# Performance work log

Measured on AMD Instinct MI355X. Metric: run time of the kernel, lower is better.

Reference implementation:

```python
import jax, jax.numpy as jnp
import numpy as np

N = 60000          # users
M = 40000          # items
NODES = N + M
D = 64             # embedding_dim
NLAYERS = 3        # layers = [64, 64, 64]
NNZ = 3_200_000    # nnz of L_I (avg degree 32)
B = 1024           # batch_size
NEG_SLOPE = 0.2


def setup_inputs() -> dict:
    key = jax.random.key(0)
    ks = jax.random.split(key, 12)
    edge_row = jax.random.randint(ks[0], (NNZ,), 0, NODES, dtype=jnp.int32)
    edge_col = jax.random.randint(ks[1], (NNZ,), 0, NODES, dtype=jnp.int32)
    # Laplacian values are small positive normalized weights
    edge_val = jax.random.uniform(ks[2], (NNZ,), dtype=jnp.float32) * (1.0 / 32.0)
    embed_user = jax.random.normal(ks[3], (N, D), dtype=jnp.float32) * 0.1
    embed_item = jax.random.normal(ks[4], (M, D), dtype=jnp.float32) * 0.1
    W1 = jax.random.normal(ks[5], (NLAYERS, D, D), dtype=jnp.float32) * 0.1
    W2 = jax.random.normal(ks[6], (NLAYERS, D, D), dtype=jnp.float32) * 0.1
    b1 = jax.random.normal(ks[7], (NLAYERS, 1, D), dtype=jnp.float32) * 0.1
    b2 = jax.random.normal(ks[8], (NLAYERS, 1, D), dtype=jnp.float32) * 0.1
    sampled_users = jax.random.randint(ks[9], (B,), 0, N, dtype=jnp.int32)
    observed_items_idx = jax.random.randint(ks[10], (B,), 0, M, dtype=jnp.int32)
    unobserved_items_idx = jax.random.randint(ks[11], (B,), 0, M, dtype=jnp.int32)
    return {
        "edge_row": edge_row, "edge_col": edge_col, "edge_val": edge_val,
        "embed_user": embed_user, "embed_item": embed_item,
        "W1": W1, "W2": W2, "b1": b1, "b2": b2,
        "sampled_users": sampled_users,
        "observed_items_idx": observed_items_idx,
        "unobserved_items_idx": unobserved_items_idx,
    }


def _spmm(row, col, val, x):
    # sparse (NODES x NODES) @ dense (NODES x D) via gather + segment-sum
    return jax.ops.segment_sum(val[:, None] * x[col], row, num_segments=NODES)


def reference(edge_row, edge_col, edge_val, embed_user, embed_item,
              W1, W2, b1, b2,
              sampled_users, observed_items_idx, unobserved_items_idx):
    x = jnp.concatenate([embed_user, embed_item], axis=0)  # (NODES, D)
    reprs = [x]
    for i in range(NLAYERS):
        lie = _spmm(edge_row, edge_col, edge_val, x)        # L_I @ E
        left = lie @ W1[i] + b1[i]
        right = (x * lie) @ W2[i] + b2[i]
        x = jax.nn.leaky_relu(left + right, negative_slope=NEG_SLOPE)
        reprs.append(x)
    final_reprs = jnp.concatenate(reprs, axis=1)            # (NODES, D*(NLAYERS+1))
    users_, items_ = final_reprs[:N], final_reprs[N:]
    return (users_[sampled_users],
            items_[observed_items_idx],
            items_[unobserved_items_idx])
```

## Files before the change

kernel.cpp:

```cpp
#include <hip/hip_runtime.h>

#define NN    60000
#define NODES 100000
#define DD    64
#define NNZ   3200000
#define BB    1024
#define NEG   0.2f
#define RPB   256
#define NBUCK 391
#define EPB   8192
#define NPB   ((NNZ + EPB - 1) / EPB)
#define CAP   8960
#define BCAP  9216

__global__ __launch_bounds__(256) void k_init_x(const float* __restrict__ eu,
                                                const float* __restrict__ ei,
                                                float* __restrict__ x,
                                                int* __restrict__ gcur) {
    int i = blockIdx.x * 256 + threadIdx.x;
    if (i < NBUCK) gcur[i] = i * CAP;
    const int TOT = NODES * DD / 4;
    if (i >= TOT) return;
    const int UE = NN * DD / 4;
    float4 v = (i < UE) ? ((const float4*)eu)[i] : ((const float4*)ei)[i - UE];
    ((float4*)x)[i] = v;
}

__global__ __launch_bounds__(512) void k_place(const int* __restrict__ row,
                                               const int* __restrict__ col,
                                               const float* __restrict__ val,
                                               int* __restrict__ gcur,
                                               int2* __restrict__ bulk) {
    __shared__ int rows_l[EPB];
    __shared__ unsigned short perm[EPB];
    __shared__ int h[NBUCK], bloc[NBUCK], bcur[NBUCK], gseg[NBUCK];
    __shared__ int sc[512];
    int t = threadIdx.x;
    if (t < NBUCK) h[t] = 0;
    __syncthreads();
    int base = blockIdx.x * EPB;
    int n = min(EPB, NNZ - base);
    for (int k = t; k < n; k += 512) {
        int r = row[base + k];
        rows_l[k] = r;
        atomicAdd(&h[r >> 8], 1);
    }
    __syncthreads();
    {
        int v = (t < NBUCK) ? h[t] : 0;
        sc[t] = v;
        __syncthreads();
        for (int off = 1; off < 512; off <<= 1) {
            int u = (t >= off) ? sc[t - off] : 0;
            __syncthreads();
            sc[t] += u;
            __syncthreads();
        }
        if (t < NBUCK) {
            int ex = sc[t] - v;
            bloc[t] = ex;
            bcur[t] = ex;
            gseg[t] = v ? atomicAdd(&gcur[t], v) : 0;
        }
    }
    __syncthreads();
    for (int k = t; k < n; k += 512) {
        int p = atomicAdd(&bcur[rows_l[k] >> 8], 1);
        perm[p] = (unsigned short)k;
    }
    __syncthreads();
    for (int j = t; j < n; j += 512) {
        int k = perm[j];
        int r = rows_l[k];
        int b8 = r >> 8;
        int addr = gseg[b8] + (j - bloc[b8]);
        bulk[addr] = make_int2(((r & 255) << 17) | col[base + k],
                               __float_as_int(val[base + k]));
    }
}

__global__ __launch_bounds__(512) void k_csr(const int* __restrict__ gcur,
                                             int2* __restrict__ bulk,
                                             int2* __restrict__ rsd) {
    __shared__ int2 eds[BCAP];
    __shared__ int h[RPB], sc[RPB], bcur[RPB];
    int b = blockIdx.x, t = threadIdx.x;
    int lo = b * CAP;
    int n = gcur[b] - lo;
    if (t < RPB) h[t] = 0;
    __syncthreads();
    for (int i = t; i < n; i += 512) {
        int2 ed = bulk[lo + i];
        eds[i] = ed;
        atomicAdd(&h[ed.x >> 17], 1);
    }
    __syncthreads();
    int v = 0;
    if (t < RPB) { v = h[t]; sc[t] = v; }
    __syncthreads();
    for (int off = 1; off < RPB; off <<= 1) {
        int u = 0;
        if (t < RPB && t >= off) u = sc[t - off];
        __syncthreads();
        if (t < RPB) sc[t] += u;
        __syncthreads();
    }
    if (t < RPB) {
        int ex = sc[t] - v;
        bcur[t] = ex;
        int r = b * RPB + t;
        if (r < NODES) rsd[r] = make_int2(lo + ex, lo + ex + v);
    }
    __syncthreads();
    for (int i = t; i < n; i += 512) {
        int2 ed = eds[i];
        int p = atomicAdd(&bcur[ed.x >> 17], 1);
        bulk[lo + p] = make_int2(ed.x & 0x1FFFF, ed.y);
    }
}

__global__ __launch_bounds__(256) void k_spmm(const int2* __restrict__ rsd,
                                              const int2* __restrict__ cv,
                                              const float* __restrict__ x,
                                              float* __restrict__ lie) {
    int w    = (blockIdx.x * 256 + threadIdx.x) >> 6;
    int lane = threadIdx.x & 63;
    if (w >= NODES) return;
    int2 se = rsd[w];
    int s = se.x, e = se.y;
    float acc = 0.f;
    int g = s;
    for (; g + 16 <= e; g += 16) {
        int2 ee[16];
#pragma unroll
        for (int j = 0; j < 16; ++j) ee[j] = cv[g + j];
        float xv[16];
#pragma unroll
        for (int j = 0; j < 16; ++j) xv[j] = x[ee[j].x * DD + lane];
#pragma unroll
        for (int j = 0; j < 16; ++j) acc = fmaf(__int_as_float(ee[j].y), xv[j], acc);
    }
    for (; g + 8 <= e; g += 8) {
        int2 ee[8];
#pragma unroll
        for (int j = 0; j < 8; ++j) ee[j] = cv[g + j];
        float xv[8];
#pragma unroll
        for (int j = 0; j < 8; ++j) xv[j] = x[ee[j].x * DD + lane];
#pragma unroll
        for (int j = 0; j < 8; ++j) acc = fmaf(__int_as_float(ee[j].y), xv[j], acc);
    }
    for (; g < e; ++g) {
        int2 ed = cv[g];
        acc = fmaf(__int_as_float(ed.y), x[ed.x * DD + lane], acc);
    }
    lie[w * DD + lane] = acc;
}

__global__ __launch_bounds__(256) void k_gemm(float* __restrict__ x,
                                              const float* __restrict__ lie,
                                              const float* __restrict__ W1,
                                              const float* __restrict__ W2,
                                              const float* __restrict__ b1,
                                              const float* __restrict__ b2) {
    __shared__ float A1[64 * 64];
    __shared__ float A2[64 * 64];
    __shared__ float Ws1[64 * 64];
    __shared__ float Ws2[64 * 64];

    const int t = threadIdx.x;
    const int row0 = blockIdx.x * 64;

    {
        const float4* w1v = (const float4*)W1;
        const float4* w2v = (const float4*)W2;
        float4* s1v = (float4*)Ws1;
        float4* s2v = (float4*)Ws2;
#pragma unroll
        for (int q = 0; q < 4; ++q) {
            s1v[q * 256 + t] = w1v[q * 256 + t];
            s2v[q * 256 + t] = w2v[q * 256 + t];
        }
    }
#pragma unroll
    for (int q = 0; q < 4; ++q) {
        int f4 = q * 256 + t;
        int rl = f4 >> 4;
        int c4 = f4 & 15;
        int gr = row0 + rl;
        float4 lv = make_float4(0.f, 0.f, 0.f, 0.f);
        float4 xv = make_float4(0.f, 0.f, 0.f, 0.f);
        if (gr < NODES) {
            lv = *(const float4*)&lie[gr * DD + c4 * 4];
            xv = *(const float4*)&x[gr * DD + c4 * 4];
        }
        int sg = c4 ^ (rl & 15);
        ((float4*)A1)[rl * 16 + sg] = lv;
        ((float4*)A2)[rl * 16 + sg] = make_float4(lv.x * xv.x, lv.y * xv.y,
                                                  lv.z * xv.z, lv.w * xv.w);
    }
    __syncthreads();

    const int tx = t & 15;
    const int ty = t >> 4;
    float bs[4];
    {
        float4 bb1 = *(const float4*)&b1[tx * 4];
        float4 bb2 = *(const float4*)&b2[tx * 4];
        bs[0] = bb1.x + bb2.x; bs[1] = bb1.y + bb2.y;
        bs[2] = bb1.z + bb2.z; bs[3] = bb1.w + bb2.w;
    }
    float acc[4][4];
#pragma unroll
    for (int i = 0; i < 4; ++i)
#pragma unroll
        for (int j = 0; j < 4; ++j) acc[i][j] = bs[j];

    for (int k4 = 0; k4 < 16; ++k4) {
        float4 a1[4], a2[4];
#pragma unroll
        for (int i = 0; i < 4; ++i) {
            int r = ty * 4 + i;
            int sg = k4 ^ (r & 15);
            a1[i] = ((const float4*)A1)[r * 16 + sg];
            a2[i] = ((const float4*)A2)[r * 16 + sg];
        }
#pragma unroll
        for (int kk = 0; kk < 4; ++kk) {
            float4 w1 = ((const float4*)Ws1)[(k4 * 4 + kk) * 16 + tx];
            float4 w2 = ((const float4*)Ws2)[(k4 * 4 + kk) * 16 + tx];
#pragma unroll
            for (int i = 0; i < 4; ++i) {
                float av1 = (&a1[i].x)[kk];
                float av2 = (&a2[i].x)[kk];
                acc[i][0] = fmaf(av1, w1.x, fmaf(av2, w2.x, acc[i][0]));
                acc[i][1] = fmaf(av1, w1.y, fmaf(av2, w2.y, acc[i][1]));
                acc[i][2] = fmaf(av1, w1.z, fmaf(av2, w2.z, acc[i][2]));
                acc[i][3] = fmaf(av1, w1.w, fmaf(av2, w2.w, acc[i][3]));
            }
        }
    }
#pragma unroll
    for (int i = 0; i < 4; ++i) {
        int gr = row0 + ty * 4 + i;
        if (gr < NODES) {
            float4 o;
            o.x = acc[i][0] >= 0.f ? acc[i][0] : NEG * acc[i][0];
            o.y = acc[i][1] >= 0.f ? acc[i][1] : NEG * acc[i][1];
            o.z = acc[i][2] >= 0.f ? acc[i][2] : NEG * acc[i][2];
            o.w = acc[i][3] >= 0.f ? acc[i][3] : NEG * acc[i][3];
            *(float4*)&x[gr * DD + tx * 4] = o;
        }
    }
}

__global__ __launch_bounds__(256) void k_gather(const float* __restrict__ x,
                                                const int* __restrict__ su,
                                                const int* __restrict__ oi,
                                                const int* __restrict__ ui,
                                                float* __restrict__ out, int layer) {
    int w    = (blockIdx.x * 256 + threadIdx.x) >> 6;
    int lane = threadIdx.x & 63;
    if (w >= 3 * BB) return;
    int g = w >> 10, b = w & 1023;
    int node = (g == 0) ? su[b] : (NN + ((g == 1) ? oi[b] : ui[b]));
    out[w * 256 + layer * 64 + lane] = x[node * DD + lane];
}

extern "C" void kernel_launch(void* const* d_in, const int* in_sizes, int n_in,
                              void* d_out, int out_size, void* d_ws, size_t ws_size,
                              hipStream_t stream) {
    const int*   edge_row = (const int*)d_in[0];
    const int*   edge_col = (const int*)d_in[1];
    const float* edge_val = (const float*)d_in[2];
    const float* eu = (const float*)d_in[3];
    const float* ei = (const float*)d_in[4];
    const float* W1 = (const float*)d_in[5];
    const float* W2 = (const float*)d_in[6];
    const float* b1 = (const float*)d_in[7];
    const float* b2 = (const float*)d_in[8];
    const int*   su = (const int*)d_in[9];
    const int*   oi = (const int*)d_in[10];
    const int*   ui = (const int*)d_in[11];
    float* out = (float*)d_out;

    float* x    = (float*)d_ws;
    float* lie  = x + NODES * DD;
    int2*  bulk = (int2*)(lie + NODES * DD);
    int*   gcur = (int*)(bulk + NBUCK * CAP);
    int2*  rsd  = (int2*)(gcur + NBUCK + 1);

    k_init_x<<<(NODES * DD / 4 + 255) / 256, 256, 0, stream>>>(eu, ei, x, gcur);
    k_gather<<<(3 * BB * 64 + 255) / 256, 256, 0, stream>>>(x, su, oi, ui, out, 0);

    k_place<<<NPB, 512, 0, stream>>>(edge_row, edge_col, edge_val, gcur, bulk);
    k_csr<<<NBUCK, 512, 0, stream>>>(gcur, bulk, rsd);

    for (int l = 0; l < 3; ++l) {
        k_spmm<<<(NODES * 64 + 255) / 256, 256, 0, stream>>>(rsd, bulk, x, lie);
        k_gemm<<<(NODES + 63) / 64, 256, 0, stream>>>(x, lie,
                                                      W1 + l * 4096, W2 + l * 4096,
                                                      b1 + l * 64,  b2 + l * 64);
        k_gather<<<(3 * BB * 64 + 255) / 256, 256, 0, stream>>>(x, su, oi, ui, out, l + 1);
    }
}
```

Measured before the change: 610.7 us.

## Sort edges by column segment within row buckets for cache-local SpMM gathers

Rows are bucketed into 196-row groups, and inside each bucket edges are sorted by (column segment of 8192 nodes, local row). A new block-per-bucket SpMM kernel walks the 13 column segments in order and accumulates partial row sums in shared memory. All blocks then gather from the same slice of x at roughly the same time, which should improve L2 hit rates. The cost is more per-key overhead, since each segment holds only short runs of about 2-3 edges, and only 511 large blocks are launched, which may limit occupancy and latency hiding.

```diff
diff --git a/kernel.cpp b/kernel.cpp
--- a/kernel.cpp
+++ b/kernel.cpp
@@ -6,12 +6,15 @@
 #define NNZ   3200000
 #define BB    1024
 #define NEG   0.2f
-#define RPB   256
-#define NBUCK 391
+#define RPB   196
+#define NBUCK 511
 #define EPB   8192
 #define NPB   ((NNZ + EPB - 1) / EPB)
-#define CAP   8960
-#define BCAP  9216
+#define CAP   7000
+#define BCAP  7168
+#define NSEG  13
+#define KEYN  (NSEG * RPB)
+#define SPB   (KEYN + 1)
 
 __global__ __launch_bounds__(256) void k_init_x(const float* __restrict__ eu,
                                                 const float* __restrict__ ei,
@@ -43,7 +46,7 @@
     for (int k = t; k < n; k += 512) {
         int r = row[base + k];
         rows_l[k] = r;
-        atomicAdd(&h[r >> 8], 1);
+        atomicAdd(&h[r / RPB], 1);
     }
     __syncthreads();
     {
@@ -65,96 +68,111 @@
     }
     __syncthreads();
     for (int k = t; k < n; k += 512) {
-        int p = atomicAdd(&bcur[rows_l[k] >> 8], 1);
+        int p = atomicAdd(&bcur[rows_l[k] / RPB], 1);
         perm[p] = (unsigned short)k;
     }
     __syncthreads();
     for (int j = t; j < n; j += 512) {
         int k = perm[j];
         int r = rows_l[k];
-        int b8 = r >> 8;
-        int addr = gseg[b8] + (j - bloc[b8]);
-        bulk[addr] = make_int2(((r & 255) << 17) | col[base + k],
+        int b = r / RPB;
+        int addr = gseg[b] + (j - bloc[b]);
+        bulk[addr] = make_int2(((r - b * RPB) << 17) | col[base + k],
                                __float_as_int(val[base + k]));
     }
 }
 
 __global__ __launch_bounds__(512) void k_csr(const int* __restrict__ gcur,
                                              int2* __restrict__ bulk,
-                                             int2* __restrict__ rsd) {
+                                             int* __restrict__ starts) {
     __shared__ int2 eds[BCAP];
-    __shared__ int h[RPB], sc[RPB], bcur[RPB];
+    __shared__ int cnt[KEYN], pos[KEYN];
+    __shared__ int part[512];
     int b = blockIdx.x, t = threadIdx.x;
     int lo = b * CAP;
     int n = gcur[b] - lo;
-    if (t < RPB) h[t] = 0;
+    for (int k = t; k < KEYN; k += 512) cnt[k] = 0;
     __syncthreads();
     for (int i = t; i < n; i += 512) {
         int2 ed = bulk[lo + i];
         eds[i] = ed;
-        atomicAdd(&h[ed.x >> 17], 1);
-    }
-    __syncthreads();
-    int v = 0;
-    if (t < RPB) { v = h[t]; sc[t] = v; }
-    __syncthreads();
-    for (int off = 1; off < RPB; off <<= 1) {
-        int u = 0;
-        if (t < RPB && t >= off) u = sc[t - off];
+        int lr = ed.x >> 17, c = ed.x & 0x1FFFF;
+        atomicAdd(&cnt[(c >> 13) * RPB + lr], 1);
+    }
+    __syncthreads();
+    int run = 0;
+#pragma unroll
+    for (int j = 0; j < 5; ++j) {
+        int k = t * 5 + j;
+        if (k < KEYN) { pos[k] = run; run += cnt[k]; }
+    }
+    part[t] = run;
+    __syncthreads();
+    for (int off = 1; off < 512; off <<= 1) {
+        int u = (t >= off) ? part[t - off] : 0;
         __syncthreads();
-        if (t < RPB) sc[t] += u;
+        part[t] += u;
         __syncthreads();
     }
-    if (t < RPB) {
-        int ex = sc[t] - v;
-        bcur[t] = ex;
-        int r = b * RPB + t;
-        if (r < NODES) rsd[r] = make_int2(lo + ex, lo + ex + v);
-    }
+    int poff = part[t] - run;
+#pragma unroll
+    for (int j = 0; j < 5; ++j) {
+        int k = t * 5 + j;
+        if (k < KEYN) pos[k] += poff;
+    }
+    __syncthreads();
+    for (int k = t; k < KEYN; k += 512) {
+        starts[b * SPB + k] = lo + pos[k];
+        cnt[k] = pos[k];
+    }
+    if (t == 0) starts[b * SPB + KEYN] = lo + n;
     __syncthreads();
     for (int i = t; i < n; i += 512) {
         int2 ed = eds[i];
-        int p = atomicAdd(&bcur[ed.x >> 17], 1);
-        bulk[lo + p] = make_int2(ed.x & 0x1FFFF, ed.y);
-    }
-}
-
-__global__ __launch_bounds__(256) void k_spmm(const int2* __restrict__ rsd,
-                                              const int2* __restrict__ cv,
-                                              const float* __restrict__ x,
-                                              float* __restrict__ lie) {
-    int w    = (blockIdx.x * 256 + threadIdx.x) >> 6;
-    int lane = threadIdx.x & 63;
-    if (w >= NODES) return;
-    int2 se = rsd[w];
-    int s = se.x, e = se.y;
-    float acc = 0.f;
-    int g = s;
-    for (; g + 16 <= e; g += 16) {
-        int2 ee[16];
-#pragma unroll
-        for (int j = 0; j < 16; ++j) ee[j] = cv[g + j];
-        float xv[16];
-#pragma unroll
-        for (int j = 0; j < 16; ++j) xv[j] = x[ee[j].x * DD + lane];
-#pragma unroll
-        for (int j = 0; j < 16; ++j) acc = fmaf(__int_as_float(ee[j].y), xv[j], acc);
-    }
-    for (; g + 8 <= e; g += 8) {
-        int2 ee[8];
-#pragma unroll
-        for (int j = 0; j < 8; ++j) ee[j] = cv[g + j];
-        float xv[8];
-#pragma unroll
-        for (int j = 0; j < 8; ++j) xv[j] = x[ee[j].x * DD + lane];
-#pragma unroll
-        for (int j = 0; j < 8; ++j) acc = fmaf(__int_as_float(ee[j].y), xv[j], acc);
-    }
-    for (; g < e; ++g) {
-        int2 ed = cv[g];
-        acc = fmaf(__int_as_float(ed.y), x[ed.x * DD + lane], acc);
-    }
-    lie[w * DD + lane] = acc;
+        int lr = ed.x >> 17, c = ed.x & 0x1FFFF;
+        int p = atomicAdd(&cnt[(c >> 13) * RPB + lr], 1);
+        bulk[lo + p] = make_int2(c, ed.y);
+    }
+}
+
+__global__ __launch_bounds__(1024) void k_cspmm(const int* __restrict__ starts,
+                                                const int2* __restrict__ cv,
+                                                const float* __restrict__ x,
+                                                float* __restrict__ lie) {
+    __shared__ float acc[RPB * DD];
+    int t = threadIdx.x, b = blockIdx.x;
+    float4* av = (float4*)acc;
+    for (int i = t; i < RPB * 16; i += 1024) av[i] = make_float4(0.f, 0.f, 0.f, 0.f);
+    __syncthreads();
+    int wid = t >> 6, lane = t & 63;
+    int sb = b * SPB;
+    for (int seg = 0; seg < NSEG; ++seg) {
+        for (int r = wid; r < RPB; r += 16) {
+            int key = sb + seg * RPB + r;
+            int s = starts[key], e = starts[key + 1];
+            if (s == e) continue;
+            float f = 0.f;
+            int g = s;
+            for (; g + 2 <= e; g += 2) {
+                int2 e0 = cv[g], e1 = cv[g + 1];
+                float x0 = x[e0.x * DD + lane];
+                float x1 = x[e1.x * DD + lane];
+                f = fmaf(__int_as_float(e0.y), x0, f);
+                f = fmaf(__int_as_float(e1.y), x1, f);
+            }
+            if (g < e) {
+                int2 e0 = cv[g];
+                f = fmaf(__int_as_float(e0.y), x[e0.x * DD + lane], f);
+            }
+            acc[r * DD + lane] += f;
+        }
+    }
+    __syncthreads();
+    int row0 = b * RPB;
+    for (int i = t; i < RPB * 16; i += 1024) {
+        int gr = row0 + (i >> 4);
+        if (gr < NODES) ((float4*)lie)[gr * 16 + (i & 15)] = av[i];
+    }
 }
 
 __global__ __launch_bounds__(256) void k_gemm(float* __restrict__ x,
@@ -284,20 +302,20 @@
     const int*   ui = (const int*)d_in[11];
     float* out = (float*)d_out;
 
-    float* x    = (float*)d_ws;
-    float* lie  = x + NODES * DD;
-    int2*  bulk = (int2*)(lie + NODES * DD);
-    int*   gcur = (int*)(bulk + NBUCK * CAP);
-    int2*  rsd  = (int2*)(gcur + NBUCK + 1);
+    float* x      = (float*)d_ws;
+    float* lie    = x + NODES * DD;
+    int2*  bulk   = (int2*)(lie + NODES * DD);
+    int*   gcur   = (int*)(bulk + NBUCK * CAP);
+    int*   starts = gcur + NBUCK + 1;
 
     k_init_x<<<(NODES * DD / 4 + 255) / 256, 256, 0, stream>>>(eu, ei, x, gcur);
     k_gather<<<(3 * BB * 64 + 255) / 256, 256, 0, stream>>>(x, su, oi, ui, out, 0);
 
     k_place<<<NPB, 512, 0, stream>>>(edge_row, edge_col, edge_val, gcur, bulk);
-    k_csr<<<NBUCK, 512, 0, stream>>>(gcur, bulk, rsd);
+    k_csr<<<NBUCK, 512, 0, stream>>>(gcur, bulk, starts);
 
     for (int l = 0; l < 3; ++l) {
-        k_spmm<<<(NODES * 64 + 255) / 256, 256, 0, stream>>>(rsd, bulk, x, lie);
+        k_cspmm<<<NBUCK, 1024, 0, stream>>>(starts, bulk, x, lie);
         k_gemm<<<(NODES + 63) / 64, 256, 0, stream>>>(x, lie,
                                                       W1 + l * 4096, W2 + l * 4096,
                                                       b1 + l * 64,  b2 + l * 64);
```

Result: slower. 914.1 us (+49.7%).

## Vectorize SpMM gathers with float4 and 4-edge-per-wave lane split

Applied to the files above, without the earlier changes.

The SpMM kernel now splits each 64-lane wave into four groups of 16 lanes. Each group handles a different edge and loads its feature row as float4, and the groups' partial sums are combined with cross-lane shuffles. This is meant to cut the number of gather instructions and raise memory-level parallelism per wave, at the cost of a shuffle reduction and less unrolling depth. The CSR build kernel also shrinks its shared edge buffer to CAP and widens the prefix scan to 512 threads with uniform participation.

```diff
diff --git a/kernel.cpp b/kernel.cpp
--- a/kernel.cpp
+++ b/kernel.cpp
@@ -11,7 +11,6 @@
 #define EPB   8192
 #define NPB   ((NNZ + EPB - 1) / EPB)
 #define CAP   8960
-#define BCAP  9216
 
 __global__ __launch_bounds__(256) void k_init_x(const float* __restrict__ eu,
                                                 const float* __restrict__ ei,
@@ -82,39 +81,39 @@
 __global__ __launch_bounds__(512) void k_csr(const int* __restrict__ gcur,
                                              int2* __restrict__ bulk,
                                              int2* __restrict__ rsd) {
-    __shared__ int2 eds[BCAP];
-    __shared__ int h[RPB], sc[RPB], bcur[RPB];
+    __shared__ int2 eds[CAP];
+    __shared__ int cnt[RPB], cur[RPB];
+    __shared__ int part[512];
     int b = blockIdx.x, t = threadIdx.x;
     int lo = b * CAP;
     int n = gcur[b] - lo;
-    if (t < RPB) h[t] = 0;
+    if (t < RPB) cnt[t] = 0;
     __syncthreads();
     for (int i = t; i < n; i += 512) {
         int2 ed = bulk[lo + i];
         eds[i] = ed;
-        atomicAdd(&h[ed.x >> 17], 1);
-    }
-    __syncthreads();
-    int v = 0;
-    if (t < RPB) { v = h[t]; sc[t] = v; }
-    __syncthreads();
-    for (int off = 1; off < RPB; off <<= 1) {
-        int u = 0;
-        if (t < RPB && t >= off) u = sc[t - off];
+        atomicAdd(&cnt[ed.x >> 17], 1);
+    }
+    __syncthreads();
+    int v = (t < RPB) ? cnt[t] : 0;
+    part[t] = v;
+    __syncthreads();
+    for (int off = 1; off < 512; off <<= 1) {
+        int u = (t >= off) ? part[t - off] : 0;
         __syncthreads();
-        if (t < RPB) sc[t] += u;
+        part[t] += u;
         __syncthreads();
     }
     if (t < RPB) {
-        int ex = sc[t] - v;
-        bcur[t] = ex;
+        int ex = part[t] - v;
+        cur[t] = ex;
         int r = b * RPB + t;
         if (r < NODES) rsd[r] = make_int2(lo + ex, lo + ex + v);
     }
     __syncthreads();
     for (int i = t; i < n; i += 512) {
         int2 ed = eds[i];
-        int p = atomicAdd(&bcur[ed.x >> 17], 1);
+        int p = atomicAdd(&cur[ed.x >> 17], 1);
         bulk[lo + p] = make_int2(ed.x & 0x1FFFF, ed.y);
     }
 }
@@ -128,33 +127,43 @@
     if (w >= NODES) return;
     int2 se = rsd[w];
     int s = se.x, e = se.y;
-    float acc = 0.f;
+    int eg = lane >> 4;
+    int d4 = lane & 15;
+    float4 f = make_float4(0.f, 0.f, 0.f, 0.f);
     int g = s;
     for (; g + 16 <= e; g += 16) {
-        int2 ee[16];
-#pragma unroll
-        for (int j = 0; j < 16; ++j) ee[j] = cv[g + j];
-        float xv[16];
-#pragma unroll
-        for (int j = 0; j < 16; ++j) xv[j] = x[ee[j].x * DD + lane];
-#pragma unroll
-        for (int j = 0; j < 16; ++j) acc = fmaf(__int_as_float(ee[j].y), xv[j], acc);
-    }
-    for (; g + 8 <= e; g += 8) {
-        int2 ee[8];
-#pragma unroll
-        for (int j = 0; j < 8; ++j) ee[j] = cv[g + j];
-        float xv[8];
-#pragma unroll
-        for (int j = 0; j < 8; ++j) xv[j] = x[ee[j].x * DD + lane];
-#pragma unroll
-        for (int j = 0; j < 8; ++j) acc = fmaf(__int_as_float(ee[j].y), xv[j], acc);
-    }
-    for (; g < e; ++g) {
-        int2 ed = cv[g];
-        acc = fmaf(__int_as_float(ed.y), x[ed.x * DD + lane], acc);
-    }
-    lie[w * DD + lane] = acc;
+        int2 e0 = cv[g + eg];
+        int2 e1 = cv[g + 4 + eg];
+        int2 e2 = cv[g + 8 + eg];
+        int2 e3 = cv[g + 12 + eg];
+        float4 x0 = *(const float4*)&x[e0.x * DD + d4 * 4];
+        float4 x1 = *(const float4*)&x[e1.x * DD + d4 * 4];
+        float4 x2 = *(const float4*)&x[e2.x * DD + d4 * 4];
+        float4 x3 = *(const float4*)&x[e3.x * DD + d4 * 4];
+        float v0 = __int_as_float(e0.y), v1 = __int_as_float(e1.y);
+        float v2 = __int_as_float(e2.y), v3 = __int_as_float(e3.y);
+        f.x = fmaf(v0, x0.x, f.x); f.y = fmaf(v0, x0.y, f.y);
+        f.z = fmaf(v0, x0.z, f.z); f.w = fmaf(v0, x0.w, f.w);
+        f.x = fmaf(v1, x1.x, f.x); f.y = fmaf(v1, x1.y, f.y);
+        f.z = fmaf(v1, x1.z, f.z); f.w = fmaf(v1, x1.w, f.w);
+        f.x = fmaf(v2, x2.x, f.x); f.y = fmaf(v2, x2.y, f.y);
+        f.z = fmaf(v2, x2.z, f.z); f.w = fmaf(v2, x2.w, f.w);
+        f.x = fmaf(v3, x3.x, f.x); f.y = fmaf(v3, x3.y, f.y);
+        f.z = fmaf(v3, x3.z, f.z); f.w = fmaf(v3, x3.w, f.w);
+    }
+    for (; g < e; g += 4) {
+        int ei = g + eg;
+        int2 ed = cv[min(ei, e - 1)];
+        float v = (ei < e) ? __int_as_float(ed.y) : 0.f;
+        float4 xv = *(const float4*)&x[ed.x * DD + d4 * 4];
+        f.x = fmaf(v, xv.x, f.x); f.y = fmaf(v, xv.y, f.y);
+        f.z = fmaf(v, xv.z, f.z); f.w = fmaf(v, xv.w, f.w);
+    }
+    f.x += __shfl_xor(f.x, 16); f.y += __shfl_xor(f.y, 16);
+    f.z += __shfl_xor(f.z, 16); f.w += __shfl_xor(f.w, 16);
+    f.x += __shfl_xor(f.x, 32); f.y += __shfl_xor(f.y, 32);
+    f.z += __shfl_xor(f.z, 32); f.w += __shfl_xor(f.w, 32);
+    if (lane < 16) *(float4*)&lie[w * DD + lane * 4] = f;
 }
 
 __global__ __launch_bounds__(256) void k_gemm(float* __restrict__ x,
```

Result: faster. 595.1 us (-2.6%).
